# Optimization experiments

Hardware: AMD Instinct MI355X
Metric: run time of the kernel (lower is better)

The kernel has to match this reference:

```python
import jax, jax.numpy as jnp
import numpy as np

B, L, H = 2, 2048, 1024
N_HEADS = 16
HEAD = H // N_HEADS
LN_EPS = 1e-12


def setup_inputs() -> dict:
    key = jax.random.key(0)
    ks = jax.random.split(key, 8)
    s = 1.0 / np.sqrt(H)
    return {
        "embeddings": jax.random.normal(ks[0], (B, L, H), dtype=jnp.float32),
        "mask": jnp.zeros((B, 1, 1, L), dtype=jnp.float32),
        "Wq": jax.random.normal(ks[1], (H, H), dtype=jnp.float32) * s,
        "bq": jnp.zeros((H,), dtype=jnp.float32),
        "Wk": jax.random.normal(ks[2], (H, H), dtype=jnp.float32) * s,
        "bk": jnp.zeros((H,), dtype=jnp.float32),
        "Wv": jax.random.normal(ks[3], (H, H), dtype=jnp.float32) * s,
        "bv": jnp.zeros((H,), dtype=jnp.float32),
        "Wo": jax.random.normal(ks[4], (H, H), dtype=jnp.float32) * s,
        "bo": jnp.zeros((H,), dtype=jnp.float32),
        "ln_gamma": jnp.ones((H,), dtype=jnp.float32),
        "ln_beta": jnp.zeros((H,), dtype=jnp.float32),
    }


def _layer_norm(x, gamma, beta):
    mu = jnp.mean(x, axis=-1, keepdims=True)
    var = jnp.mean(jnp.square(x - mu), axis=-1, keepdims=True)
    return (x - mu) * jax.lax.rsqrt(var + LN_EPS) * gamma + beta


def reference(embeddings, mask, Wq, bq, Wk, bk, Wv, bv, Wo, bo, ln_gamma, ln_beta):
    b, l, h = embeddings.shape
    # QKV projections, split heads -> [b, n_heads, l, head]
    def split_heads(x):
        return x.reshape(b, l, N_HEADS, HEAD).transpose(0, 2, 1, 3)
    q = split_heads(embeddings @ Wq + bq)
    k = split_heads(embeddings @ Wk + bk)
    v = split_heads(embeddings @ Wv + bv)
    # Faithful to source: energies use Q @ V^T, scaled by sqrt(n_heads)
    energies = jnp.einsum("bhqd,bhkd->bhqk", q, v) / np.sqrt(N_HEADS) + mask
    weights = jax.nn.softmax(energies, axis=3)
    # Faithful to source: attended = weights @ K
    attended = jnp.einsum("bhqk,bhkd->bhqd", weights, k)
    attended = attended.transpose(0, 2, 1, 3).reshape(b, l, h)
    # Residual feed-forward (BertSelfOutput style): dense + residual + LN
    out = attended @ Wo + bo
    return _layer_norm(out + embeddings, ln_gamma, ln_beta)
```

## Files before the change

kernel.cpp:

```cpp
#include <hip/hip_runtime.h>

#define LOG2E 1.44269504f
#define C_QSCALE 0.360673760f
#define C_SHIFT  34.6246810f
typedef unsigned short u16;
typedef short bf16x8 __attribute__((ext_vector_type(8)));
typedef float f32x4 __attribute__((ext_vector_type(4)));
typedef unsigned short u16x4 __attribute__((ext_vector_type(4)));

#define BB 2
#define LL 2048
#define HH 1024
#define NH 16
#define HD 64
#define ML (BB*LL)

__device__ __forceinline__ u16 f2bf(float f) {
  union { float f; unsigned u; } v; v.f = f;
  unsigned r = v.u + 0x7FFFu + ((v.u >> 16) & 1u);
  return (u16)(r >> 16);
}
__device__ __forceinline__ u16 f2bf_trunc(float f) {
  union { float f; unsigned u; } v; v.f = f;
  return (u16)(v.u >> 16);
}
__device__ __forceinline__ float bf2f(u16 u) {
  union { unsigned u; float f; } v; v.u = ((unsigned)u) << 16;
  return v.f;
}
__device__ __forceinline__ void gload_lds16(const u16* g, u16* l) {
  __builtin_amdgcn_global_load_lds((const __attribute__((address_space(1))) void*)g,
                                   (__attribute__((address_space(3))) void*)l, 16, 0, 0);
}

__global__ __launch_bounds__(256) void k_prep(const float* __restrict__ E, u16* __restrict__ X,
                                              const float* W0, const float* W1,
                                              const float* W2, const float* W3,
                                              u16* __restrict__ WT) {
  __shared__ __align__(16) u16 T[64*72];
  if (blockIdx.x < 2048) {
    int idx = (blockIdx.x * 256 + threadIdx.x) * 8;
    float4 a = *(const float4*)(E + idx);
    float4 b = *(const float4*)(E + idx + 4);
    bf16x8 o;
    o[0]=f2bf(a.x); o[1]=f2bf(a.y); o[2]=f2bf(a.z); o[3]=f2bf(a.w);
    o[4]=f2bf(b.x); o[5]=f2bf(b.y); o[6]=f2bf(b.z); o[7]=f2bf(b.w);
    *(bf16x8*)(X + idx) = o;
    return;
  }
  int bz = blockIdx.x - 2048;
  int z = bz >> 8, rem = bz & 255, bx = rem & 15, by = rem >> 4;
  const float* W = (z==0)?W0:(z==1)?W1:(z==2)?W2:W3;
  u16* dst = WT + (size_t)z * HH * HH;
  int t = threadIdx.x;
  int n0 = bx * 64, k0 = by * 64;
  int kl = t >> 2, nc = t & 3;
  #pragma unroll
  for (int u = 0; u < 4; ++u) {
    float4 v = *(const float4*)(W + (size_t)(k0 + kl) * HH + n0 + nc*16 + u*4);
    int nb = nc*16 + u*4;
    T[(nb+0)*72 + kl] = f2bf(v.x);
    T[(nb+1)*72 + kl] = f2bf(v.y);
    T[(nb+2)*72 + kl] = f2bf(v.z);
    T[(nb+3)*72 + kl] = f2bf(v.w);
  }
  __syncthreads();
  int nl = t >> 2, kc = (t & 3) * 16;
  #pragma unroll
  for (int e = 0; e < 2; ++e) {
    bf16x8 v = *(const bf16x8*)(T + nl*72 + kc + e*8);
    *(bf16x8*)(dst + (size_t)(n0+nl)*HH + k0 + kc + e*8) = v;
  }
}

__global__ __launch_bounds__(256) void k_gemm(const u16* __restrict__ A, const u16* __restrict__ Bt,
                                              const float* __restrict__ b0, const float* __restrict__ b1,
                                              const float* __restrict__ b2,
                                              u16* __restrict__ QH, u16* __restrict__ KV) {
  __shared__ __align__(16) u16 As[2][128*32];
  __shared__ __align__(16) u16 Bs[2][128*32];
  int tid = threadIdx.x;
  int lane = tid & 63, w = tid >> 6;
  int c = lane & 15, g = lane >> 4;
  int bn0 = blockIdx.x * 128, bm0 = blockIdx.y * 128;
  int wm0 = (w >> 1) * 64, wn0 = (w & 1) * 64;
  int z = bn0 >> 10;
  bool swapd = (z != 1);
  const u16* srcA = swapd ? Bt : A;
  const u16* srcB = swapd ? A : Bt;
  int baseA = swapd ? bn0 : bm0;
  int baseB = swapd ? bm0 : bn0;

  f32x4 acc[4][4];
  #pragma unroll
  for (int mt = 0; mt < 4; ++mt)
    #pragma unroll
    for (int nt = 0; nt < 4; ++nt)
      acc[mt][nt] = (f32x4){0.f,0.f,0.f,0.f};

  #pragma unroll
  for (int it = 0; it < 2; ++it) {
    int ch = tid + it*256, row = ch >> 2, col = (ch & 3) * 8;
    gload_lds16(srcA + (size_t)(baseA + row) * HH + col, &As[0][ch*8]);
    gload_lds16(srcB + (size_t)(baseB + row) * HH + col, &Bs[0][ch*8]);
  }
  for (int kt = 0; kt < 32; ++kt) {
    __syncthreads();
    int cb = kt & 1;
    if (kt < 31) {
      int k0 = (kt + 1) * 32, nb = (kt + 1) & 1;
      #pragma unroll
      for (int it = 0; it < 2; ++it) {
        int ch = tid + it*256, row = ch >> 2, col = (ch & 3) * 8;
        gload_lds16(srcA + (size_t)(baseA + row) * HH + k0 + col, &As[nb][ch*8]);
        gload_lds16(srcB + (size_t)(baseB + row) * HH + k0 + col, &Bs[nb][ch*8]);
      }
    }
    bf16x8 af[4], bfr[4];
    #pragma unroll
    for (int i = 0; i < 4; ++i) {
      af[i]  = *(const bf16x8*)(&As[cb][0] + (wm0 + i*16 + c)*32 + g*8);
      bfr[i] = *(const bf16x8*)(&Bs[cb][0] + (wn0 + i*16 + c)*32 + g*8);
    }
    #pragma unroll
    for (int mt = 0; mt < 4; ++mt)
      #pragma unroll
      for (int nt = 0; nt < 4; ++nt)
        acc[mt][nt] = __builtin_amdgcn_mfma_f32_16x16x32_bf16(af[mt], bfr[nt], acc[mt][nt], 0, 0, 0);
  }

  if (z == 1) {
    #pragma unroll
    for (int nt = 0; nt < 4; ++nt) {
      int n = bn0 + wn0 + nt*16 + c;
      int nn = n & 1023, h = nn >> 6, d = nn & 63;
      float bv = b1[nn];
      #pragma unroll
      for (int mt = 0; mt < 4; ++mt) {
        int m0 = bm0 + wm0 + mt*16 + 4*g;
        int b = m0 >> 11, keyl = m0 & 2047;
        int tt = keyl >> 6, chunk = (keyl >> 3) & 7, s = keyl & 7;
        u16x4 pk;
        #pragma unroll
        for (int r = 0; r < 4; ++r) pk[r] = f2bf(acc[mt][nt][r] + bv);
        *(u16x4*)(KV + ((size_t)((b*NH + h)*32 + tt))*8192 + d*64 + ((chunk ^ (d & 7))*8) + s) = pk;
      }
    }
  } else {
    #pragma unroll
    for (int mt = 0; mt < 4; ++mt) {
      int nidx0 = bn0 + wm0 + mt*16 + 4*g;
      int nn0 = nidx0 & 1023, h = nn0 >> 6, d0 = nn0 & 63;
      const float* bp = (z == 0) ? b0 : b2;
      float4 bv = *(const float4*)(bp + nn0);
      #pragma unroll
      for (int nt = 0; nt < 4; ++nt) {
        int tok = bm0 + wn0 + nt*16 + c;
        int b = tok >> 11, l = tok & 2047;
        u16x4 o;
        o[0] = f2bf(acc[mt][nt][0] + bv.x);
        o[1] = f2bf(acc[mt][nt][1] + bv.y);
        o[2] = f2bf(acc[mt][nt][2] + bv.z);
        o[3] = f2bf(acc[mt][nt][3] + bv.w);
        if (z == 0) {
          *(u16x4*)(QH + (((size_t)(b*NH + h)) * LL + l) * HD + d0) = o;
        } else {
          int tt = l >> 6;
          *(u16x4*)(KV + ((size_t)((b*NH + h)*32 + tt))*8192 + 4096
                    + (l & 63)*64 + (((d0 >> 3) ^ (l & 7))*8) + (d0 & 7)) = o;
        }
      }
    }
  }
}

__global__ __launch_bounds__(256) void k_gemm_o(const u16* __restrict__ ATT, const u16* __restrict__ Wt,
                                                const float* __restrict__ bias,
                                                float* __restrict__ outf) {
  __shared__ __align__(16) u16 As[2][128*32];
  __shared__ __align__(16) u16 Bs[2][64*32];
  int tid = threadIdx.x;
  int lane = tid & 63, w = tid >> 6;
  int c = lane & 15, g = lane >> 4;
  int bn0 = blockIdx.x * 128, bm0 = blockIdx.y * 64;
  int wm0 = (w >> 1) * 64, wn0 = (w & 1) * 32;

  f32x4 acc[4][2];
  #pragma unroll
  for (int mt = 0; mt < 4; ++mt)
    #pragma unroll
    for (int nt = 0; nt < 2; ++nt)
      acc[mt][nt] = (f32x4){0.f,0.f,0.f,0.f};

  #pragma unroll
  for (int it = 0; it < 2; ++it) {
    int ch = tid + it*256, row = ch >> 2, col = (ch & 3) * 8;
    gload_lds16(Wt + (size_t)(bn0 + row) * HH + col, &As[0][ch*8]);
  }
  { int row = tid >> 2, col = (tid & 3) * 8;
    gload_lds16(ATT + (size_t)(bm0 + row) * HH + col, &Bs[0][tid*8]); }

  for (int kt = 0; kt < 32; ++kt) {
    __syncthreads();
    int cb = kt & 1;
    if (kt < 31) {
      int k0 = (kt + 1) * 32, nb = (kt + 1) & 1;
      #pragma unroll
      for (int it = 0; it < 2; ++it) {
        int ch = tid + it*256, row = ch >> 2, col = (ch & 3) * 8;
        gload_lds16(Wt + (size_t)(bn0 + row) * HH + k0 + col, &As[nb][ch*8]);
      }
      int row = tid >> 2, col = (tid & 3) * 8;
      gload_lds16(ATT + (size_t)(bm0 + row) * HH + k0 + col, &Bs[nb][tid*8]);
    }
    bf16x8 af[4], bfr[2];
    #pragma unroll
    for (int i = 0; i < 4; ++i)
      af[i] = *(const bf16x8*)(&As[cb][0] + (wm0 + i*16 + c)*32 + g*8);
    #pragma unroll
    for (int j = 0; j < 2; ++j)
      bfr[j] = *(const bf16x8*)(&Bs[cb][0] + (wn0 + j*16 + c)*32 + g*8);
    #pragma unroll
    for (int mt = 0; mt < 4; ++mt)
      #pragma unroll
      for (int nt = 0; nt < 2; ++nt)
        acc[mt][nt] = __builtin_amdgcn_mfma_f32_16x16x32_bf16(af[mt], bfr[nt], acc[mt][nt], 0, 0, 0);
  }
  #pragma unroll
  for (int mt = 0; mt < 4; ++mt) {
    int n0 = bn0 + wm0 + mt*16 + 4*g;
    float4 bv = *(const float4*)(bias + n0);
    #pragma unroll
    for (int nt = 0; nt < 2; ++nt) {
      int tok = bm0 + wn0 + nt*16 + c;
      float4 o;
      o.x = acc[mt][nt][0] + bv.x;
      o.y = acc[mt][nt][1] + bv.y;
      o.z = acc[mt][nt][2] + bv.z;
      o.w = acc[mt][nt][3] + bv.w;
      *(float4*)(outf + (size_t)tok * HH + n0) = o;
    }
  }
}

__global__ __launch_bounds__(256) void k_attn(const u16* __restrict__ QH, const u16* __restrict__ KV,
                                              const float* __restrict__ mask,
                                              u16* __restrict__ PO, float* __restrict__ PL) {
  __shared__ __align__(16) u16 sKV[2][8192];
  __shared__ __align__(16) u16 sP[4][32*72];
  int tid = threadIdx.x;
  int lane = tid & 63, w = tid >> 6;
  int c = lane & 15, g = lane >> 4;
  int z = blockIdx.y;
  int bh = blockIdx.z, b = bh >> 4;
  int q0 = blockIdx.x * 128 + w * 32;
  size_t qbase = (size_t)bh * LL * HD;
  const u16* kvg = KV + (size_t)bh * 32 * 8192 + (size_t)z * 16 * 8192;
  const float* mptr = mask + b * LL + z * 1024;
  u16* pw = &sP[w][0];

  bf16x8 aq[2][2];
  #pragma unroll
  for (int qi = 0; qi < 2; ++qi)
    #pragma unroll
    for (int ks = 0; ks < 2; ++ks)
      aq[qi][ks] = *(const bf16x8*)(QH + qbase + (size_t)(q0 + qi*16 + c) * HD + ks*32 + g*8);

  bf16x8 ones;
  #pragma unroll
  for (int i = 0; i < 8; ++i) ones[i] = (short)0x3F80;

  f32x4 O[2][4], lac[2];
  #pragma unroll
  for (int qi = 0; qi < 2; ++qi) {
    lac[qi] = (f32x4){0.f,0.f,0.f,0.f};
    #pragma unroll
    for (int dt = 0; dt < 4; ++dt) O[qi][dt] = (f32x4){0.f,0.f,0.f,0.f};
  }

  #pragma unroll
  for (int it = 0; it < 4; ++it) {
    int i = (tid + it*256) * 8;
    gload_lds16(kvg + i, &sKV[0][0] + i);
  }
  for (int tt = 0; tt < 16; ++tt) {
    __syncthreads();
    const u16* cur = &sKV[tt & 1][0];
    if (tt < 15) {
      const u16* src = kvg + (size_t)(tt + 1) * 8192;
      u16* dst = &sKV[(tt + 1) & 1][0];
      #pragma unroll
      for (int it = 0; it < 4; ++it) {
        int i = (tid + it*256) * 8;
        gload_lds16(src + i, dst + i);
      }
    }
    int kv0 = tt * 64;
    #pragma unroll
    for (int nt = 0; nt < 4; ++nt) {
      int vrow = nt*16 + c;
      bf16x8 vb0 = *(const bf16x8*)(cur + 4096 + vrow*64 + ((g ^ (c & 7))*8));
      bf16x8 vb1 = *(const bf16x8*)(cur + 4096 + vrow*64 + (((4 + g) ^ (c & 7))*8));
      float mterm = fmaf(mptr[kv0 + vrow], LOG2E, -C_SHIFT);
      #pragma unroll
      for (int qi = 0; qi < 2; ++qi) {
        f32x4 sa = (f32x4){0.f,0.f,0.f,0.f};
        sa = __builtin_amdgcn_mfma_f32_16x16x32_bf16(aq[qi][0], vb0, sa, 0,0,0);
        sa = __builtin_amdgcn_mfma_f32_16x16x32_bf16(aq[qi][1], vb1, sa, 0,0,0);
        #pragma unroll
        for (int r = 0; r < 4; ++r)
          pw[(qi*16 + 4*g + r)*72 + nt*16 + c] = f2bf_trunc(exp2f(fmaf(sa[r], C_QSCALE, mterm)));
      }
    }
    bf16x8 ap[2][2];
    #pragma unroll
    for (int qi = 0; qi < 2; ++qi) {
      ap[qi][0] = *(const bf16x8*)(pw + (qi*16 + c)*72 + g*8);
      ap[qi][1] = *(const bf16x8*)(pw + (qi*16 + c)*72 + 32 + g*8);
      lac[qi] = __builtin_amdgcn_mfma_f32_16x16x32_bf16(ones, ap[qi][0], lac[qi], 0,0,0);
      lac[qi] = __builtin_amdgcn_mfma_f32_16x16x32_bf16(ones, ap[qi][1], lac[qi], 0,0,0);
    }
    #pragma unroll
    for (int dt = 0; dt < 4; ++dt) {
      int d = dt*16 + c;
      bf16x8 bk0 = *(const bf16x8*)(cur + d*64 + ((g ^ (c & 7))*8));
      bf16x8 bk1 = *(const bf16x8*)(cur + d*64 + (((4 + g) ^ (c & 7))*8));
      #pragma unroll
      for (int qi = 0; qi < 2; ++qi) {
        O[qi][dt] = __builtin_amdgcn_mfma_f32_16x16x32_bf16(bk0, ap[qi][0], O[qi][dt], 0,0,0);
        O[qi][dt] = __builtin_amdgcn_mfma_f32_16x16x32_bf16(bk1, ap[qi][1], O[qi][dt], 0,0,0);
      }
    }
  }
  #pragma unroll
  for (int qi = 0; qi < 2; ++qi) {
    size_t qrow = (size_t)(z*32 + bh) * LL + q0 + qi*16 + c;
    if (g == 0) PL[qrow] = lac[qi][0];
    #pragma unroll
    for (int dt = 0; dt < 4; ++dt) {
      u16x4 o;
      #pragma unroll
      for (int r = 0; r < 4; ++r) o[r] = f2bf(O[qi][dt][r]);
      *(u16x4*)(PO + qrow*HD + dt*16 + 4*g) = o;
    }
  }
}

__global__ __launch_bounds__(256) void k_combine(const u16* __restrict__ PO,
                                                 const float* __restrict__ PL,
                                                 u16* __restrict__ ATT) {
  int bh = blockIdx.y, b = bh >> 4, h = bh & 15;
  int q = blockIdx.x * 128 + (threadIdx.x >> 1);
  int dh = (threadIdx.x & 1) * 32;
  size_t r0 = ((size_t)bh * LL + q) * HD + dh;
  size_t r1 = ((size_t)(32 + bh) * LL + q) * HD + dh;
  float inv = 1.0f / (PL[(size_t)bh * LL + q] + PL[(size_t)(32 + bh) * LL + q]);
  u16* dst = ATT + ((size_t)(b*LL + q)) * HH + h*HD + dh;
  #pragma unroll
  for (int e = 0; e < 4; ++e) {
    bf16x8 a = *(const bf16x8*)(PO + r0 + e*8);
    bf16x8 bb = *(const bf16x8*)(PO + r1 + e*8);
    bf16x8 o;
    #pragma unroll
    for (int i = 0; i < 8; ++i)
      o[i] = (short)f2bf((bf2f((u16)a[i]) + bf2f((u16)bb[i])) * inv);
    *(bf16x8*)(dst + e*8) = o;
  }
}

__global__ __launch_bounds__(256) void k_ln(const float* __restrict__ OF, const float* __restrict__ E,
                                            const float* __restrict__ gamma, const float* __restrict__ beta,
                                            float* __restrict__ out) {
  int row = blockIdx.x;
  int tid = threadIdx.x, lane = tid & 63, w = tid >> 6;
  size_t basei = (size_t)row * HH + tid*4;
  float4 a = *(const float4*)(OF + basei);
  float4 e = *(const float4*)(E + basei);
  float x0 = a.x + e.x, x1 = a.y + e.y, x2 = a.z + e.z, x3 = a.w + e.w;
  float s1 = x0+x1+x2+x3;
  float s2 = x0*x0+x1*x1+x2*x2+x3*x3;
  #pragma unroll
  for (int off = 32; off; off >>= 1) { s1 += __shfl_xor(s1, off); s2 += __shfl_xor(s2, off); }
  __shared__ float r1[4], r2[4];
  if (lane == 0) { r1[w] = s1; r2[w] = s2; }
  __syncthreads();
  s1 = r1[0]+r1[1]+r1[2]+r1[3];
  s2 = r2[0]+r2[1]+r2[2]+r2[3];
  float mu = s1 * (1.0f/HH);
  float var = s2 * (1.0f/HH) - mu*mu;
  float rs = rsqrtf(fmaxf(var, 0.f) + 1e-12f);
  int colb = tid*4;
  float4 gm = *(const float4*)(gamma + colb);
  float4 bt = *(const float4*)(beta + colb);
  float4 o;
  o.x = (x0-mu)*rs*gm.x + bt.x;
  o.y = (x1-mu)*rs*gm.y + bt.y;
  o.z = (x2-mu)*rs*gm.z + bt.z;
  o.w = (x3-mu)*rs*gm.w + bt.w;
  *(float4*)(out + basei) = o;
}

extern "C" void kernel_launch(void* const* d_in, const int* in_sizes, int n_in,
                              void* d_out, int out_size, void* d_ws, size_t ws_size,
                              hipStream_t stream) {
  const float* E    = (const float*)d_in[0];
  const float* mask = (const float*)d_in[1];
  const float* Wq   = (const float*)d_in[2];
  const float* bq   = (const float*)d_in[3];
  const float* Wk   = (const float*)d_in[4];
  const float* bk   = (const float*)d_in[5];
  const float* Wv   = (const float*)d_in[6];
  const float* bv   = (const float*)d_in[7];
  const float* Wo   = (const float*)d_in[8];
  const float* bo   = (const float*)d_in[9];
  const float* gam  = (const float*)d_in[10];
  const float* bet  = (const float*)d_in[11];

  const size_t MH = (size_t)ML * HH;
  u16* XBF = (u16*)d_ws;
  u16* WT  = XBF + MH;
  u16* QH  = WT + 4*(size_t)HH*HH;
  u16* KV  = QH + MH;
  u16* ATT = KV + 2*MH;
  u16* PO  = ATT + MH;
  float* PL = (float*)XBF;
  float* OF = (float*)PO;
  float* out = (float*)d_out;

  k_prep<<<dim3(3072), 256, 0, stream>>>(E, XBF, Wq, Wk, Wv, Wo, WT);
  k_gemm<<<dim3(24,32), 256, 0, stream>>>(XBF, WT, bq, bk, bv, QH, KV);
  k_attn<<<dim3(16,2,32), 256, 0, stream>>>(QH, KV, mask, PO, PL);
  k_combine<<<dim3(16,32), 256, 0, stream>>>(PO, PL, ATT);
  k_gemm_o<<<dim3(8,64), 256, 0, stream>>>(ATT, WT + 3*(size_t)HH*HH, bo, OF);
  k_ln<<<dim3(ML), 256, 0, stream>>>(OF, E, gam, bet, out);
}
```

Measured before the change: 249.3 us.

## Split attention KV range three ways with single-buffered LDS and smaller P scratch

Attention blocks now split the 32 KV tiles into three chunks (11/11/10) instead of two, raising grid size, and each writes to its own partial output buffer. The KV tile is single-buffered with two barriers per tile, and the two query sub-tiles are processed sequentially to halve P scratch, cutting LDS use to allow more resident blocks. The combine kernel sums three partials, and scratch buffers are re-aliased onto dead input/output storage. The trade-off is loss of load/compute overlap and extra combine traffic.

```diff
diff --git a/kernel.cpp b/kernel.cpp
--- a/kernel.cpp
+++ b/kernel.cpp
@@ -245,9 +245,10 @@
 
 __global__ __launch_bounds__(256) void k_attn(const u16* __restrict__ QH, const u16* __restrict__ KV,
                                               const float* __restrict__ mask,
-                                              u16* __restrict__ PO, float* __restrict__ PL) {
-  __shared__ __align__(16) u16 sKV[2][8192];
-  __shared__ __align__(16) u16 sP[4][32*72];
+                                              u16* __restrict__ PO0, u16* __restrict__ PO1,
+                                              u16* __restrict__ PO2, float* __restrict__ PL) {
+  __shared__ __align__(16) u16 sKV[8192];
+  __shared__ __align__(16) u16 sP[4][16*72];
   int tid = threadIdx.x;
   int lane = tid & 63, w = tid >> 6;
   int c = lane & 15, g = lane >> 4;
@@ -255,9 +256,11 @@
   int bh = blockIdx.z, b = bh >> 4;
   int q0 = blockIdx.x * 128 + w * 32;
   size_t qbase = (size_t)bh * LL * HD;
-  const u16* kvg = KV + (size_t)bh * 32 * 8192 + (size_t)z * 16 * 8192;
-  const float* mptr = mask + b * LL + z * 1024;
+  const u16* kvg = KV + (size_t)bh * 32 * 8192;
+  const float* mptr = mask + b * LL;
   u16* pw = &sP[w][0];
+  int t0 = (z < 2) ? z*11 : 22;
+  int tn = (z < 2) ? 11 : 10;
 
   bf16x8 aq[2][2];
   #pragma unroll
@@ -278,92 +281,87 @@
     for (int dt = 0; dt < 4; ++dt) O[qi][dt] = (f32x4){0.f,0.f,0.f,0.f};
   }
 
-  #pragma unroll
-  for (int it = 0; it < 4; ++it) {
-    int i = (tid + it*256) * 8;
-    gload_lds16(kvg + i, &sKV[0][0] + i);
-  }
-  for (int tt = 0; tt < 16; ++tt) {
+  for (int ti = 0; ti < tn; ++ti) {
+    int t = t0 + ti;
     __syncthreads();
-    const u16* cur = &sKV[tt & 1][0];
-    if (tt < 15) {
-      const u16* src = kvg + (size_t)(tt + 1) * 8192;
-      u16* dst = &sKV[(tt + 1) & 1][0];
-      #pragma unroll
-      for (int it = 0; it < 4; ++it) {
-        int i = (tid + it*256) * 8;
-        gload_lds16(src + i, dst + i);
-      }
-    }
-    int kv0 = tt * 64;
-    #pragma unroll
-    for (int nt = 0; nt < 4; ++nt) {
-      int vrow = nt*16 + c;
-      bf16x8 vb0 = *(const bf16x8*)(cur + 4096 + vrow*64 + ((g ^ (c & 7))*8));
-      bf16x8 vb1 = *(const bf16x8*)(cur + 4096 + vrow*64 + (((4 + g) ^ (c & 7))*8));
-      float mterm = fmaf(mptr[kv0 + vrow], LOG2E, -C_SHIFT);
-      #pragma unroll
-      for (int qi = 0; qi < 2; ++qi) {
+    #pragma unroll
+    for (int it = 0; it < 4; ++it) {
+      int i = (tid + it*256) * 8;
+      gload_lds16(kvg + (size_t)t*8192 + i, sKV + i);
+    }
+    __syncthreads();
+
+    int kv0 = t * 64;
+    float mt4[4];
+    #pragma unroll
+    for (int nt = 0; nt < 4; ++nt)
+      mt4[nt] = fmaf(mptr[kv0 + nt*16 + c], LOG2E, -C_SHIFT);
+
+    #pragma unroll
+    for (int qi = 0; qi < 2; ++qi) {
+      #pragma unroll
+      for (int nt = 0; nt < 4; ++nt) {
+        int vrow = nt*16 + c;
+        bf16x8 vb0 = *(const bf16x8*)(sKV + 4096 + vrow*64 + ((g ^ (c & 7))*8));
+        bf16x8 vb1 = *(const bf16x8*)(sKV + 4096 + vrow*64 + (((4 + g) ^ (c & 7))*8));
         f32x4 sa = (f32x4){0.f,0.f,0.f,0.f};
         sa = __builtin_amdgcn_mfma_f32_16x16x32_bf16(aq[qi][0], vb0, sa, 0,0,0);
         sa = __builtin_amdgcn_mfma_f32_16x16x32_bf16(aq[qi][1], vb1, sa, 0,0,0);
         #pragma unroll
         for (int r = 0; r < 4; ++r)
-          pw[(qi*16 + 4*g + r)*72 + nt*16 + c] = f2bf_trunc(exp2f(fmaf(sa[r], C_QSCALE, mterm)));
-      }
-    }
-    bf16x8 ap[2][2];
-    #pragma unroll
-    for (int qi = 0; qi < 2; ++qi) {
-      ap[qi][0] = *(const bf16x8*)(pw + (qi*16 + c)*72 + g*8);
-      ap[qi][1] = *(const bf16x8*)(pw + (qi*16 + c)*72 + 32 + g*8);
-      lac[qi] = __builtin_amdgcn_mfma_f32_16x16x32_bf16(ones, ap[qi][0], lac[qi], 0,0,0);
-      lac[qi] = __builtin_amdgcn_mfma_f32_16x16x32_bf16(ones, ap[qi][1], lac[qi], 0,0,0);
-    }
-    #pragma unroll
-    for (int dt = 0; dt < 4; ++dt) {
-      int d = dt*16 + c;
-      bf16x8 bk0 = *(const bf16x8*)(cur + d*64 + ((g ^ (c & 7))*8));
-      bf16x8 bk1 = *(const bf16x8*)(cur + d*64 + (((4 + g) ^ (c & 7))*8));
-      #pragma unroll
-      for (int qi = 0; qi < 2; ++qi) {
-        O[qi][dt] = __builtin_amdgcn_mfma_f32_16x16x32_bf16(bk0, ap[qi][0], O[qi][dt], 0,0,0);
-        O[qi][dt] = __builtin_amdgcn_mfma_f32_16x16x32_bf16(bk1, ap[qi][1], O[qi][dt], 0,0,0);
-      }
-    }
-  }
+          pw[(4*g + r)*72 + nt*16 + c] = f2bf_trunc(exp2f(fmaf(sa[r], C_QSCALE, mt4[nt])));
+      }
+      bf16x8 ap0 = *(const bf16x8*)(pw + c*72 + g*8);
+      bf16x8 ap1 = *(const bf16x8*)(pw + c*72 + 32 + g*8);
+      lac[qi] = __builtin_amdgcn_mfma_f32_16x16x32_bf16(ones, ap0, lac[qi], 0,0,0);
+      lac[qi] = __builtin_amdgcn_mfma_f32_16x16x32_bf16(ones, ap1, lac[qi], 0,0,0);
+      #pragma unroll
+      for (int dt = 0; dt < 4; ++dt) {
+        int d = dt*16 + c;
+        bf16x8 bk0 = *(const bf16x8*)(sKV + d*64 + ((g ^ (c & 7))*8));
+        bf16x8 bk1 = *(const bf16x8*)(sKV + d*64 + (((4 + g) ^ (c & 7))*8));
+        O[qi][dt] = __builtin_amdgcn_mfma_f32_16x16x32_bf16(bk0, ap0, O[qi][dt], 0,0,0);
+        O[qi][dt] = __builtin_amdgcn_mfma_f32_16x16x32_bf16(bk1, ap1, O[qi][dt], 0,0,0);
+      }
+    }
+  }
+  u16* POp = (z == 0) ? PO0 : (z == 1) ? PO1 : PO2;
   #pragma unroll
   for (int qi = 0; qi < 2; ++qi) {
-    size_t qrow = (size_t)(z*32 + bh) * LL + q0 + qi*16 + c;
-    if (g == 0) PL[qrow] = lac[qi][0];
+    int q = q0 + qi*16 + c;
+    size_t qrow = (size_t)bh * LL + q;
+    if (g == 0) PL[(size_t)(z*32 + bh) * LL + q] = lac[qi][0];
     #pragma unroll
     for (int dt = 0; dt < 4; ++dt) {
       u16x4 o;
       #pragma unroll
       for (int r = 0; r < 4; ++r) o[r] = f2bf(O[qi][dt][r]);
-      *(u16x4*)(PO + qrow*HD + dt*16 + 4*g) = o;
-    }
-  }
-}
-
-__global__ __launch_bounds__(256) void k_combine(const u16* __restrict__ PO,
+      *(u16x4*)(POp + qrow*HD + dt*16 + 4*g) = o;
+    }
+  }
+}
+
+__global__ __launch_bounds__(256) void k_combine(const u16* __restrict__ PO0,
+                                                 const u16* __restrict__ PO1,
+                                                 const u16* __restrict__ PO2,
                                                  const float* __restrict__ PL,
                                                  u16* __restrict__ ATT) {
   int bh = blockIdx.y, b = bh >> 4, h = bh & 15;
   int q = blockIdx.x * 128 + (threadIdx.x >> 1);
   int dh = (threadIdx.x & 1) * 32;
   size_t r0 = ((size_t)bh * LL + q) * HD + dh;
-  size_t r1 = ((size_t)(32 + bh) * LL + q) * HD + dh;
-  float inv = 1.0f / (PL[(size_t)bh * LL + q] + PL[(size_t)(32 + bh) * LL + q]);
+  float inv = 1.0f / (PL[(size_t)bh * LL + q] + PL[(size_t)(32 + bh) * LL + q]
+                    + PL[(size_t)(64 + bh) * LL + q]);
   u16* dst = ATT + ((size_t)(b*LL + q)) * HH + h*HD + dh;
   #pragma unroll
   for (int e = 0; e < 4; ++e) {
-    bf16x8 a = *(const bf16x8*)(PO + r0 + e*8);
-    bf16x8 bb = *(const bf16x8*)(PO + r1 + e*8);
+    bf16x8 a0 = *(const bf16x8*)(PO0 + r0 + e*8);
+    bf16x8 a1 = *(const bf16x8*)(PO1 + r0 + e*8);
+    bf16x8 a2 = *(const bf16x8*)(PO2 + r0 + e*8);
     bf16x8 o;
     #pragma unroll
     for (int i = 0; i < 8; ++i)
-      o[i] = (short)f2bf((bf2f((u16)a[i]) + bf2f((u16)bb[i])) * inv);
+      o[i] = (short)f2bf((bf2f((u16)a0[i]) + bf2f((u16)a1[i]) + bf2f((u16)a2[i])) * inv);
     *(bf16x8*)(dst + e*8) = o;
   }
 }
@@ -422,15 +420,17 @@
   u16* QH  = WT + 4*(size_t)HH*HH;
   u16* KV  = QH + MH;
   u16* ATT = KV + 2*MH;
-  u16* PO  = ATT + MH;
-  float* PL = (float*)XBF;
-  float* OF = (float*)PO;
+  u16* PO0 = ATT + MH;
+  u16* PO1 = PO0 + MH;
+  u16* PO2 = XBF;
   float* out = (float*)d_out;
+  float* PL = out;
+  float* OF = (float*)PO0;
 
   k_prep<<<dim3(3072), 256, 0, stream>>>(E, XBF, Wq, Wk, Wv, Wo, WT);
   k_gemm<<<dim3(24,32), 256, 0, stream>>>(XBF, WT, bq, bk, bv, QH, KV);
-  k_attn<<<dim3(16,2,32), 256, 0, stream>>>(QH, KV, mask, PO, PL);
-  k_combine<<<dim3(16,32), 256, 0, stream>>>(PO, PL, ATT);
+  k_attn<<<dim3(16,3,32), 256, 0, stream>>>(QH, KV, mask, PO0, PO1, PO2, PL);
+  k_combine<<<dim3(16,32), 256, 0, stream>>>(PO0, PO1, PO2, PL, ATT);
   k_gemm_o<<<dim3(8,64), 256, 0, stream>>>(ATT, WT + 3*(size_t)HH*HH, bo, OF);
   k_ln<<<dim3(ML), 256, 0, stream>>>(OF, E, gam, bet, out);
 }
```

New measurement: 253.6 us. About the same (+1.7%).
